# Performance work log

Hardware: AMD Instinct MI355X
Metric: run time of the kernel (lower is better)

Reference implementation:

```python
import jax, jax.numpy as jnp
import numpy as np

THETA = 10000.0


def _apply_rope(xh, positions, theta):
    # xh: [B, H, S, d_k]; positions: [S] int
    d_k = xh.shape[-1]
    inv_freq = theta ** (-jnp.arange(0, d_k, 2, dtype=jnp.float32) / d_k)  # [d_k/2]
    angles = positions.astype(jnp.float32)[:, None] * inv_freq[None, :]     # [S, d_k/2]
    cos = jnp.cos(angles)
    sin = jnp.sin(angles)
    x1 = xh[..., 0::2]
    x2 = xh[..., 1::2]
    r1 = x1 * cos - x2 * sin
    r2 = x1 * sin + x2 * cos
    return jnp.stack([r1, r2], axis=-1).reshape(xh.shape)


def setup_inputs() -> dict:
    key = jax.random.key(0)
    ks = jax.random.split(key, 5)
    B, S, D = 2, 2048, 1024
    std = np.sqrt(1.0 / D).astype(np.float32)
    return {
        "x": jax.random.normal(ks[0], (B, S, D), dtype=jnp.float32),
        "token_positions": jnp.arange(S, dtype=jnp.int64 if jax.config.jax_enable_x64 else jnp.int32),
        "Wq": jax.random.normal(ks[1], (D, D), dtype=jnp.float32) * std,
        "Wk": jax.random.normal(ks[2], (D, D), dtype=jnp.float32) * std,
        "Wv": jax.random.normal(ks[3], (D, D), dtype=jnp.float32) * std,
        "Wo": jax.random.normal(ks[4], (D, D), dtype=jnp.float32) * std,
    }


def reference(x, token_positions, Wq, Wk, Wv, Wo):
    B, S, D = x.shape
    n_heads = 16
    d_k = D // n_heads

    # QKV projections (torch does x @ W.T)
    q = x @ Wq.T
    k = x @ Wk.T
    v = x @ Wv.T

    def split_heads(t):  # [B,S,D] -> [B,H,S,d_k]
        return t.reshape(B, S, n_heads, d_k).transpose(0, 2, 1, 3)

    qh = _apply_rope(split_heads(q), token_positions, THETA)
    kh = _apply_rope(split_heads(k), token_positions, THETA)
    vh = split_heads(v)

    scores = jnp.einsum("bhqd,bhkd->bhqk", qh, kh) / jnp.sqrt(jnp.float32(d_k))
    causal = jnp.tril(jnp.ones((S, S), dtype=bool))
    scores = jnp.where(causal, scores, -jnp.inf)
    attn = jax.nn.softmax(scores, axis=-1)

    out_h = jnp.einsum("bhqk,bhkd->bhqd", attn, vh)  # [B,H,S,d_k]
    out = out_h.transpose(0, 2, 1, 3).reshape(B, S, D)
    return out @ Wo.T
```

## Files before the change

kernel.cpp:

```cpp
#include <hip/hip_runtime.h>

typedef unsigned int u32;
typedef __attribute__((ext_vector_type(8))) short short8;
typedef __attribute__((ext_vector_type(4))) float f32x4;

__device__ __forceinline__ unsigned short f2bf(float f) {
  union { float f; u32 u; } x; x.f = f;
  u32 u = x.u;
  return (unsigned short)((u + 0x7fffu + ((u >> 16) & 1u)) >> 16);
}
__device__ __forceinline__ float bf2f(unsigned short b) {
  union { u32 u; float f; } x; x.u = ((u32)b) << 16;
  return x.f;
}
__device__ __forceinline__ f32x4 mfma_bf16(short8 a, short8 b, f32x4 c) {
  return __builtin_amdgcn_mfma_f32_16x16x32_bf16(a, b, c, 0, 0, 0);
}

typedef __attribute__((address_space(3))) unsigned int lds_u32;
typedef const __attribute__((address_space(1))) unsigned int glb_u32;
__device__ __forceinline__ void gload_lds16(const unsigned short* g, unsigned short* l) {
  __builtin_amdgcn_global_load_lds((glb_u32*)g, (lds_u32*)l, 16, 0, 0);
}

__global__ __launch_bounds__(256) void cvt_kernel(const float* __restrict__ src,
                                                  unsigned short* __restrict__ dst, int n4) {
  int i = blockIdx.x * 256 + threadIdx.x;
  if (i >= n4) return;
  float4 v = ((const float4*)src)[i];
  ushort4 o;
  o.x = f2bf(v.x); o.y = f2bf(v.y); o.z = f2bf(v.z); o.w = f2bf(v.w);
  ((ushort4*)dst)[i] = o;
}

__global__ __launch_bounds__(256) void cvt_w_kernel(const float* __restrict__ wq,
                                                    const float* __restrict__ wk,
                                                    const float* __restrict__ wv,
                                                    const float* __restrict__ wo,
                                                    unsigned short* __restrict__ dqkv,
                                                    unsigned short* __restrict__ dwo) {
  const int i = blockIdx.x * 256 + threadIdx.x;
  const int w = blockIdx.y;
  const float* src = (w == 0) ? wq : (w == 1) ? wk : (w == 2) ? wv : wo;
  unsigned short* dst = (w == 3) ? dwo : dqkv + (size_t)w * 1048576;
  float4 v = ((const float4*)src)[i];
  ushort4 o;
  o.x = f2bf(v.x); o.y = f2bf(v.y); o.z = f2bf(v.z); o.w = f2bf(v.w);
  ((ushort4*)dst)[i] = o;
}

__global__ __launch_bounds__(256) void gemm_qkv(const unsigned short* __restrict__ A,
                                                const unsigned short* __restrict__ B,
                                                unsigned short* __restrict__ qk,
                                                unsigned short* __restrict__ kk,
                                                unsigned short* __restrict__ vtm) {
  constexpr int K = 1024;
  __shared__ unsigned short As[128 * 32];
  __shared__ unsigned short Bs[128 * 32];
  const int tid = threadIdx.x;
  const int wave = tid >> 6, lane = tid & 63;
  const int l15 = lane & 15, quad = lane >> 4;
  const int wr = wave >> 1, wc = wave & 1;
  const int m0 = blockIdx.y * 128, n0 = blockIdx.x * 128;
  f32x4 acc[4][4] = {};
  const int srow = wave * 32 + (lane >> 2);
  const int scol = (lane & 3) * 8;
  const unsigned short* Ag0 = A + (size_t)(m0 + srow) * K + scol;
  const unsigned short* Ag1 = A + (size_t)(m0 + srow + 16) * K + scol;
  const unsigned short* Bg0 = B + (size_t)(n0 + srow) * K + scol;
  const unsigned short* Bg1 = B + (size_t)(n0 + srow + 16) * K + scol;
  unsigned short* Al0 = &As[wave * 1024];
  unsigned short* Al1 = &As[wave * 1024 + 512];
  unsigned short* Bl0 = &Bs[wave * 1024];
  unsigned short* Bl1 = &Bs[wave * 1024 + 512];
  for (int k0 = 0; k0 < K; k0 += 32) {
    __syncthreads();
    gload_lds16(Ag0 + k0, Al0);
    gload_lds16(Ag1 + k0, Al1);
    gload_lds16(Bg0 + k0, Bl0);
    gload_lds16(Bg1 + k0, Bl1);
    __syncthreads();
    short8 a[4], b[4];
#pragma unroll
    for (int i = 0; i < 4; ++i) a[i] = *(const short8*)&As[(wr * 64 + i * 16 + l15) * 32 + quad * 8];
#pragma unroll
    for (int j = 0; j < 4; ++j) b[j] = *(const short8*)&Bs[(wc * 64 + j * 16 + l15) * 32 + quad * 8];
#pragma unroll
    for (int i = 0; i < 4; ++i)
#pragma unroll
      for (int j = 0; j < 4; ++j) acc[i][j] = mfma_bf16(a[i], b[j], acc[i][j]);
  }
  const int proj = n0 >> 10;
  const int nn0 = (n0 & 1023) + wc * 64;
  if (proj < 2) {
    unsigned short* dst = (proj == 0) ? qk : kk;
#pragma unroll
    for (int i = 0; i < 4; ++i) {
      const int mb = m0 + wr * 64 + i * 16 + quad * 4;
#pragma unroll
      for (int j = 0; j < 4; ++j) {
        const int nn = nn0 + j * 16 + l15;
#pragma unroll
        for (int r = 0; r < 4; ++r) dst[(size_t)(mb + r) * 1024 + nn] = f2bf(acc[i][j][r]);
      }
    }
  } else {
#pragma unroll
    for (int i = 0; i < 4; ++i) {
      const int mb = m0 + wr * 64 + i * 16 + quad * 4;
      const int bb = mb >> 11, s = mb & 2047;
#pragma unroll
      for (int j = 0; j < 4; ++j) {
        const int nn = nn0 + j * 16 + l15;
        const int h = nn >> 6, d = nn & 63;
        ushort4 v4;
        v4.x = f2bf(acc[i][j][0]); v4.y = f2bf(acc[i][j][1]);
        v4.z = f2bf(acc[i][j][2]); v4.w = f2bf(acc[i][j][3]);
        *(ushort4*)&vtm[(((size_t)bb * 16 + h) * 64 + d) * 2048 + s] = v4;
      }
    }
  }
}

__global__ __launch_bounds__(256) void rope_kernel(unsigned short* __restrict__ q,
                                                   unsigned short* __restrict__ k,
                                                   const int* __restrict__ pos) {
  const int idx = blockIdx.x * 256 + threadIdx.x;
  const int i = idx & 31;
  const int h = (idx >> 5) & 15;
  const int s = (idx >> 9) & 2047;
  const int b = idx >> 20;
  const float p = (float)pos[s];
  const float inv = exp2f(-0.4152410118609203f * (float)i);
  float sn, cs;
  sincosf(p * inv, &sn, &cs);
  const size_t base = ((size_t)(b * 2048 + s)) * 1024 + h * 64 + 2 * i;
  {
    u32* qp = (u32*)(q + base);
    u32 w = *qp;
    float x1 = bf2f((unsigned short)(w & 0xffff)), x2 = bf2f((unsigned short)(w >> 16));
    *qp = (u32)f2bf(x1 * cs - x2 * sn) | ((u32)f2bf(x1 * sn + x2 * cs) << 16);
  }
  {
    u32* kp = (u32*)(k + base);
    u32 w = *kp;
    float x1 = bf2f((unsigned short)(w & 0xffff)), x2 = bf2f((unsigned short)(w >> 16));
    *kp = (u32)f2bf(x1 * cs - x2 * sn) | ((u32)f2bf(x1 * sn + x2 * cs) << 16);
  }
}

__global__ __launch_bounds__(64) void attn_kernel(const unsigned short* __restrict__ qk,
                                                  const unsigned short* __restrict__ kk,
                                                  const unsigned short* __restrict__ vtm,
                                                  unsigned short* __restrict__ om) {
  __shared__ unsigned short Pl[32 * 72];
  const int lane = threadIdx.x;
  const int l15 = lane & 15, quad = lane >> 4;
  const int bid = blockIdx.x;
  const int bh = bid & 31;
  const int qi = 63 - (bid >> 5);
  const int b = bh >> 4, h = bh & 15;
  const int qbase = qi << 5;
  const unsigned short* Qp = qk + (size_t)b * 2048 * 1024 + h * 64;
  const unsigned short* Kp = kk + (size_t)b * 2048 * 1024 + h * 64;
  const unsigned short* Vp = vtm + (size_t)bh * 64 * 2048;
  short8 qf[2][2];
#pragma unroll
  for (int f = 0; f < 2; ++f)
#pragma unroll
    for (int hh = 0; hh < 2; ++hh)
      qf[f][hh] = *(const short8*)(Qp + (size_t)(qbase + f * 16 + l15) * 1024 + hh * 32 + quad * 8);
  f32x4 o4[2][4] = {};
  f32x4 ls[2] = {};
  short8 ones;
#pragma unroll
  for (int j = 0; j < 8; ++j) ones[j] = (short)0x3F80;
  const float SC = 0.18033688011112042f;
  const int nk = (qbase + 95) >> 6;
  for (int kt = 0; kt < nk; ++kt) {
    const int kbase = kt << 6;
    short8 kb[4][2], vb[4][2];
#pragma unroll
    for (int nt = 0; nt < 4; ++nt)
#pragma unroll
      for (int hh = 0; hh < 2; ++hh)
        kb[nt][hh] = *(const short8*)(Kp + (size_t)(kbase + nt * 16 + l15) * 1024 + hh * 32 + quad * 8);
#pragma unroll
    for (int t = 0; t < 4; ++t)
#pragma unroll
      for (int hh = 0; hh < 2; ++hh)
        vb[t][hh] = *(const short8*)(Vp + (size_t)(t * 16 + l15) * 2048 + kbase + hh * 32 + quad * 8);
    f32x4 s4[2][4] = {};
#pragma unroll
    for (int f = 0; f < 2; ++f)
#pragma unroll
      for (int nt = 0; nt < 4; ++nt) {
        s4[f][nt] = mfma_bf16(qf[f][0], kb[nt][0], s4[f][nt]);
        s4[f][nt] = mfma_bf16(qf[f][1], kb[nt][1], s4[f][nt]);
      }
    const bool edge = (kt == nk - 1);
#pragma unroll
    for (int f = 0; f < 2; ++f) {
      const int row0 = qbase + f * 16 + quad * 4;
#pragma unroll
      for (int nt = 0; nt < 4; ++nt) {
        const int col = kbase + nt * 16 + l15;
#pragma unroll
        for (int r = 0; r < 4; ++r) {
          float p = exp2f(s4[f][nt][r] * SC);
          if (edge && col > row0 + r) p = 0.f;
          Pl[(f * 16 + quad * 4 + r) * 72 + nt * 16 + l15] = f2bf(p);
        }
      }
    }
    __asm volatile("s_waitcnt lgkmcnt(0)" ::: "memory");
    short8 pa[2][2];
#pragma unroll
    for (int f = 0; f < 2; ++f)
#pragma unroll
      for (int hh = 0; hh < 2; ++hh)
        pa[f][hh] = *(const short8*)&Pl[(f * 16 + l15) * 72 + hh * 32 + quad * 8];
#pragma unroll
    for (int f = 0; f < 2; ++f) {
#pragma unroll
      for (int t = 0; t < 4; ++t) {
        o4[f][t] = mfma_bf16(pa[f][0], vb[t][0], o4[f][t]);
        o4[f][t] = mfma_bf16(pa[f][1], vb[t][1], o4[f][t]);
      }
      ls[f] = mfma_bf16(pa[f][0], ones, ls[f]);
      ls[f] = mfma_bf16(pa[f][1], ones, ls[f]);
    }
  }
#pragma unroll
  for (int f = 0; f < 2; ++f) {
    f32x4 rl;
#pragma unroll
    for (int r = 0; r < 4; ++r) rl[r] = 1.f / ls[f][r];
#pragma unroll
    for (int t = 0; t < 4; ++t)
#pragma unroll
      for (int r = 0; r < 4; ++r) {
        const int srow = qbase + f * 16 + quad * 4 + r;
        om[((size_t)b * 2048 + srow) * 1024 + h * 64 + t * 16 + l15] = f2bf(o4[f][t][r] * rl[r]);
      }
  }
}

__global__ __launch_bounds__(256) void gemm_out(const unsigned short* __restrict__ A,
                                                const unsigned short* __restrict__ B,
                                                float* __restrict__ C) {
  constexpr int K = 1024;
  __shared__ unsigned short As[64 * 32];
  __shared__ unsigned short Bs[128 * 32];
  const int tid = threadIdx.x;
  const int wave = tid >> 6, lane = tid & 63;
  const int l15 = lane & 15, quad = lane >> 4;
  const int m0 = blockIdx.y * 64, n0 = blockIdx.x * 128;
  f32x4 acc[4][2] = {};
  const int lr = lane >> 2, lc = (lane & 3) * 8;
  const unsigned short* Ag  = A + (size_t)(m0 + wave * 16 + lr) * K + lc;
  const unsigned short* Bg0 = B + (size_t)(n0 + wave * 32 + lr) * K + lc;
  const unsigned short* Bg1 = B + (size_t)(n0 + wave * 32 + 16 + lr) * K + lc;
  unsigned short* Al  = &As[wave * 512];
  unsigned short* Bl0 = &Bs[wave * 1024];
  unsigned short* Bl1 = &Bs[wave * 1024 + 512];
  for (int k0 = 0; k0 < K; k0 += 32) {
    __syncthreads();
    gload_lds16(Ag + k0, Al);
    gload_lds16(Bg0 + k0, Bl0);
    gload_lds16(Bg1 + k0, Bl1);
    __syncthreads();
    short8 a[4], b[2];
#pragma unroll
    for (int i = 0; i < 4; ++i) a[i] = *(const short8*)&As[(i * 16 + l15) * 32 + quad * 8];
#pragma unroll
    for (int j = 0; j < 2; ++j) b[j] = *(const short8*)&Bs[(wave * 32 + j * 16 + l15) * 32 + quad * 8];
#pragma unroll
    for (int i = 0; i < 4; ++i)
#pragma unroll
      for (int j = 0; j < 2; ++j) acc[i][j] = mfma_bf16(a[i], b[j], acc[i][j]);
  }
#pragma unroll
  for (int i = 0; i < 4; ++i)
#pragma unroll
    for (int j = 0; j < 2; ++j)
#pragma unroll
      for (int r = 0; r < 4; ++r)
        C[(size_t)(m0 + i * 16 + quad * 4 + r) * 1024 + n0 + wave * 32 + j * 16 + l15] =
            acc[i][j][r];
}

extern "C" void kernel_launch(void* const* d_in, const int* in_sizes, int n_in,
                              void* d_out, int out_size, void* d_ws, size_t ws_size,
                              hipStream_t stream) {
  const float* x  = (const float*)d_in[0];
  const int* pos  = (const int*)d_in[1];
  const float* Wq = (const float*)d_in[2];
  const float* Wk = (const float*)d_in[3];
  const float* Wv = (const float*)d_in[4];
  const float* Wo = (const float*)d_in[5];
  float* out = (float*)d_out;
  char* ws = (char*)d_ws;
  unsigned short* xb   = (unsigned short*)(ws);
  unsigned short* wqkv = (unsigned short*)(ws + (size_t)( 8 << 20));
  unsigned short* wob  = (unsigned short*)(ws + (size_t)(14 << 20));
  unsigned short* qkb  = (unsigned short*)(ws + (size_t)(16 << 20));
  unsigned short* kkb  = (unsigned short*)(ws + (size_t)(24 << 20));
  unsigned short* vtm  = (unsigned short*)(ws + (size_t)(32 << 20));
  unsigned short* om   = (unsigned short*)(ws + (size_t)(40 << 20));

  const int NX4 = 4096 * 1024 / 4;
  hipLaunchKernelGGL(cvt_kernel, dim3(NX4 / 256), dim3(256), 0, stream, x, xb, NX4);
  hipLaunchKernelGGL(cvt_w_kernel, dim3(1024, 4), dim3(256), 0, stream, Wq, Wk, Wv, Wo, wqkv, wob);

  hipLaunchKernelGGL(gemm_qkv, dim3(24, 32), dim3(256), 0, stream, xb, wqkv, qkb, kkb, vtm);
  hipLaunchKernelGGL(rope_kernel, dim3(8192), dim3(256), 0, stream, qkb, kkb, pos);
  hipLaunchKernelGGL(attn_kernel, dim3(2048), dim3(64), 0, stream, qkb, kkb, vtm, om);
  hipLaunchKernelGGL(gemm_out, dim3(8, 64), dim3(256), 0, stream, om, wob, out);
}
```

Measured before the change: 237.7 us.

## Split key range across two waves per attention block and combine partials in LDS

Each attention block now runs two waves, each processing half of the causal key tiles for the same 32 query rows, then wave 1 writes its unnormalized output and row-sum accumulators to shared memory for wave 0 to add and normalize. This shortens the serial key loop per block and doubles the waves available to hide memory latency. It adds two block barriers, an LDS exchange, and idle time when the halves are unequal.

```diff
diff --git a/kernel.cpp b/kernel.cpp
--- a/kernel.cpp
+++ b/kernel.cpp
@@ -149,13 +149,15 @@
   }
 }
 
-__global__ __launch_bounds__(64) void attn_kernel(const unsigned short* __restrict__ qk,
-                                                  const unsigned short* __restrict__ kk,
-                                                  const unsigned short* __restrict__ vtm,
-                                                  unsigned short* __restrict__ om) {
-  __shared__ unsigned short Pl[32 * 72];
-  const int lane = threadIdx.x;
+__global__ __launch_bounds__(128, 4) void attn_kernel(const unsigned short* __restrict__ qk,
+                                                      const unsigned short* __restrict__ kk,
+                                                      const unsigned short* __restrict__ vtm,
+                                                      unsigned short* __restrict__ om) {
+  __shared__ f32x4 cmb[640];
+  const int tid = threadIdx.x;
+  const int wave = tid >> 6, lane = tid & 63;
   const int l15 = lane & 15, quad = lane >> 4;
+  unsigned short* Pl = (unsigned short*)cmb + wave * 2304;
   const int bid = blockIdx.x;
   const int bh = bid & 31;
   const int qi = 63 - (bid >> 5);
@@ -177,7 +179,10 @@
   for (int j = 0; j < 8; ++j) ones[j] = (short)0x3F80;
   const float SC = 0.18033688011112042f;
   const int nk = (qbase + 95) >> 6;
-  for (int kt = 0; kt < nk; ++kt) {
+  const int half = (nk + 1) >> 1;
+  const int k0w = wave * half;
+  const int k1w = (wave == 0) ? half : nk;
+  for (int kt = k0w; kt < k1w; ++kt) {
     const int kbase = kt << 6;
     short8 kb[4][2], vb[4][2];
 #pragma unroll
@@ -231,18 +236,34 @@
       ls[f] = mfma_bf16(pa[f][1], ones, ls[f]);
     }
   }
-#pragma unroll
-  for (int f = 0; f < 2; ++f) {
-    f32x4 rl;
-#pragma unroll
-    for (int r = 0; r < 4; ++r) rl[r] = 1.f / ls[f][r];
-#pragma unroll
-    for (int t = 0; t < 4; ++t)
-#pragma unroll
-      for (int r = 0; r < 4; ++r) {
-        const int srow = qbase + f * 16 + quad * 4 + r;
-        om[((size_t)b * 2048 + srow) * 1024 + h * 64 + t * 16 + l15] = f2bf(o4[f][t][r] * rl[r]);
-      }
+  __syncthreads();
+  if (wave == 1) {
+#pragma unroll
+    for (int f = 0; f < 2; ++f) {
+#pragma unroll
+      for (int t = 0; t < 4; ++t) cmb[(f * 4 + t) * 64 + lane] = o4[f][t];
+      cmb[512 + f * 64 + lane] = ls[f];
+    }
+  }
+  __syncthreads();
+  if (wave == 0) {
+#pragma unroll
+    for (int f = 0; f < 2; ++f) {
+      f32x4 lw = cmb[512 + f * 64 + lane];
+      f32x4 lt;
+#pragma unroll
+      for (int r = 0; r < 4; ++r) lt[r] = 1.f / (ls[f][r] + lw[r]);
+#pragma unroll
+      for (int t = 0; t < 4; ++t) {
+        f32x4 ow = cmb[(f * 4 + t) * 64 + lane];
+#pragma unroll
+        for (int r = 0; r < 4; ++r) {
+          const int srow = qbase + f * 16 + quad * 4 + r;
+          om[((size_t)b * 2048 + srow) * 1024 + h * 64 + t * 16 + l15] =
+              f2bf((o4[f][t][r] + ow[r]) * lt[r]);
+        }
+      }
+    }
   }
 }
 
@@ -315,6 +336,6 @@
 
   hipLaunchKernelGGL(gemm_qkv, dim3(24, 32), dim3(256), 0, stream, xb, wqkv, qkb, kkb, vtm);
   hipLaunchKernelGGL(rope_kernel, dim3(8192), dim3(256), 0, stream, qkb, kkb, pos);
-  hipLaunchKernelGGL(attn_kernel, dim3(2048), dim3(64), 0, stream, qkb, kkb, vtm, om);
+  hipLaunchKernelGGL(attn_kernel, dim3(2048), dim3(128), 0, stream, qkb, kkb, vtm, om);
   hipLaunchKernelGGL(gemm_out, dim3(8, 64), dim3(256), 0, stream, om, wob, out);
 }
```

Result: slower. 264.7 us (+11.4%).

## Split attention KV range across two blocks and combine partial outputs

Applied to the files above, without the earlier changes.

Adds a split-K attention variant in which each query tile's key range is divided into two halves handled by separate blocks. Each block writes unnormalized fp32 partial outputs and row sums, and a combine kernel adds them and normalizes into bf16. The aim is more parallelism and better load balance across CUs for the causal workload. The cost is an extra kernel launch and about 32MB of fp32 intermediate traffic. It relies on exp2 without max subtraction, matching the existing kernel's numerics, and only runs when the workspace is large enough.

```diff
diff --git a/kernel.cpp b/kernel.cpp
--- a/kernel.cpp
+++ b/kernel.cpp
@@ -149,6 +149,135 @@
   }
 }
 
+__global__ __launch_bounds__(64, 4) void attn_split(const unsigned short* __restrict__ qk,
+                                                    const unsigned short* __restrict__ kk,
+                                                    const unsigned short* __restrict__ vtm,
+                                                    float* __restrict__ op,
+                                                    float* __restrict__ lsum) {
+  __shared__ unsigned short Pl[32 * 72];
+  const int lane = threadIdx.x;
+  const int l15 = lane & 15, quad = lane >> 4;
+  const int bid = blockIdx.x;
+  const int split = bid >> 11;
+  const int rem = bid & 2047;
+  const int bh = rem & 31;
+  const int qi = 63 - (rem >> 5);
+  const int b = bh >> 4, h = bh & 15;
+  const int qbase = qi << 5;
+  const unsigned short* Qp = qk + (size_t)b * 2048 * 1024 + h * 64;
+  const unsigned short* Kp = kk + (size_t)b * 2048 * 1024 + h * 64;
+  const unsigned short* Vp = vtm + (size_t)bh * 64 * 2048;
+  short8 qf[2][2];
+#pragma unroll
+  for (int f = 0; f < 2; ++f)
+#pragma unroll
+    for (int hh = 0; hh < 2; ++hh)
+      qf[f][hh] = *(const short8*)(Qp + (size_t)(qbase + f * 16 + l15) * 1024 + hh * 32 + quad * 8);
+  f32x4 o4[2][4] = {};
+  f32x4 ls[2] = {};
+  short8 ones;
+#pragma unroll
+  for (int j = 0; j < 8; ++j) ones[j] = (short)0x3F80;
+  const float SC = 0.18033688011112042f;
+  const int nk = (qbase + 95) >> 6;
+  const int half = (nk + 1) >> 1;
+  const int kts = split * half;
+  const int kte = split ? nk : half;
+  for (int kt = kts; kt < kte; ++kt) {
+    const int kbase = kt << 6;
+    short8 kb[4][2], vb[4][2];
+#pragma unroll
+    for (int nt = 0; nt < 4; ++nt)
+#pragma unroll
+      for (int hh = 0; hh < 2; ++hh)
+        kb[nt][hh] = *(const short8*)(Kp + (size_t)(kbase + nt * 16 + l15) * 1024 + hh * 32 + quad * 8);
+#pragma unroll
+    for (int t = 0; t < 4; ++t)
+#pragma unroll
+      for (int hh = 0; hh < 2; ++hh)
+        vb[t][hh] = *(const short8*)(Vp + (size_t)(t * 16 + l15) * 2048 + kbase + hh * 32 + quad * 8);
+    f32x4 s4[2][4] = {};
+#pragma unroll
+    for (int f = 0; f < 2; ++f)
+#pragma unroll
+      for (int nt = 0; nt < 4; ++nt) {
+        s4[f][nt] = mfma_bf16(qf[f][0], kb[nt][0], s4[f][nt]);
+        s4[f][nt] = mfma_bf16(qf[f][1], kb[nt][1], s4[f][nt]);
+      }
+    const bool edge = (kt == nk - 1);
+#pragma unroll
+    for (int f = 0; f < 2; ++f) {
+      const int row0 = qbase + f * 16 + quad * 4;
+#pragma unroll
+      for (int nt = 0; nt < 4; ++nt) {
+        const int col = kbase + nt * 16 + l15;
+#pragma unroll
+        for (int r = 0; r < 4; ++r) {
+          float p = exp2f(s4[f][nt][r] * SC);
+          if (edge && col > row0 + r) p = 0.f;
+          Pl[(f * 16 + quad * 4 + r) * 72 + nt * 16 + l15] = f2bf(p);
+        }
+      }
+    }
+    __asm volatile("s_waitcnt lgkmcnt(0)" ::: "memory");
+    short8 pa[2][2];
+#pragma unroll
+    for (int f = 0; f < 2; ++f)
+#pragma unroll
+      for (int hh = 0; hh < 2; ++hh)
+        pa[f][hh] = *(const short8*)&Pl[(f * 16 + l15) * 72 + hh * 32 + quad * 8];
+#pragma unroll
+    for (int f = 0; f < 2; ++f) {
+#pragma unroll
+      for (int t = 0; t < 4; ++t) {
+        o4[f][t] = mfma_bf16(pa[f][0], vb[t][0], o4[f][t]);
+        o4[f][t] = mfma_bf16(pa[f][1], vb[t][1], o4[f][t]);
+      }
+      ls[f] = mfma_bf16(pa[f][0], ones, ls[f]);
+      ls[f] = mfma_bf16(pa[f][1], ones, ls[f]);
+    }
+  }
+  float* opp = op + (size_t)split * 4096 * 1024;
+#pragma unroll
+  for (int f = 0; f < 2; ++f)
+#pragma unroll
+    for (int t = 0; t < 4; ++t)
+#pragma unroll
+      for (int r = 0; r < 4; ++r) {
+        const int srow = qbase + f * 16 + quad * 4 + r;
+        opp[((size_t)b * 2048 + srow) * 1024 + h * 64 + t * 16 + l15] = o4[f][t][r];
+      }
+  if (l15 == 0) {
+#pragma unroll
+    for (int f = 0; f < 2; ++f)
+#pragma unroll
+      for (int r = 0; r < 4; ++r) {
+        const int srow = qbase + f * 16 + quad * 4 + r;
+        lsum[((((size_t)split * 2 + b) * 16 + h) * 2048) + srow] = ls[f][r];
+      }
+  }
+}
+
+__global__ __launch_bounds__(256) void attn_combine(const float* __restrict__ op,
+                                                    const float* __restrict__ lsum,
+                                                    unsigned short* __restrict__ om) {
+  const int i = blockIdx.x * 256 + threadIdx.x;
+  const int row = i >> 8;
+  const int b = row >> 11, s = row & 2047;
+  const int h = (i & 255) >> 4;
+  float4 a0 = ((const float4*)op)[i];
+  float4 a1 = ((const float4*)(op + (size_t)4096 * 1024))[i];
+  const float l0 = lsum[((size_t)b * 16 + h) * 2048 + s];
+  const float l1 = lsum[(((size_t)2 + b) * 16 + h) * 2048 + s];
+  const float rl = 1.f / (l0 + l1);
+  ushort4 o;
+  o.x = f2bf((a0.x + a1.x) * rl);
+  o.y = f2bf((a0.y + a1.y) * rl);
+  o.z = f2bf((a0.z + a1.z) * rl);
+  o.w = f2bf((a0.w + a1.w) * rl);
+  ((ushort4*)om)[i] = o;
+}
+
 __global__ __launch_bounds__(64) void attn_kernel(const unsigned short* __restrict__ qk,
                                                   const unsigned short* __restrict__ kk,
                                                   const unsigned short* __restrict__ vtm,
@@ -308,6 +437,8 @@
   unsigned short* kkb  = (unsigned short*)(ws + (size_t)(24 << 20));
   unsigned short* vtm  = (unsigned short*)(ws + (size_t)(32 << 20));
   unsigned short* om   = (unsigned short*)(ws + (size_t)(40 << 20));
+  float* op   = (float*)(ws + (size_t)(48 << 20));
+  float* lsum = (float*)(ws + (size_t)(80 << 20));
 
   const int NX4 = 4096 * 1024 / 4;
   hipLaunchKernelGGL(cvt_kernel, dim3(NX4 / 256), dim3(256), 0, stream, x, xb, NX4);
@@ -315,6 +446,11 @@
 
   hipLaunchKernelGGL(gemm_qkv, dim3(24, 32), dim3(256), 0, stream, xb, wqkv, qkb, kkb, vtm);
   hipLaunchKernelGGL(rope_kernel, dim3(8192), dim3(256), 0, stream, qkb, kkb, pos);
-  hipLaunchKernelGGL(attn_kernel, dim3(2048), dim3(64), 0, stream, qkb, kkb, vtm, om);
+  if (ws_size >= ((size_t)81 << 20)) {
+    hipLaunchKernelGGL(attn_split, dim3(4096), dim3(64), 0, stream, qkb, kkb, vtm, op, lsum);
+    hipLaunchKernelGGL(attn_combine, dim3(4096), dim3(256), 0, stream, op, lsum, om);
+  } else {
+    hipLaunchKernelGGL(attn_kernel, dim3(2048), dim3(64), 0, stream, qkb, kkb, vtm, om);
+  }
   hipLaunchKernelGGL(gemm_out, dim3(8, 64), dim3(256), 0, stream, om, wob, out);
 }
```

Result: slower. 245.8 us (+3.4%).

## Share K/V tiles across four waves via LDS in attention kernel

Applied to the files above, without the earlier changes.

The attention kernel now runs four waves per block, each handling a 32-row query slice of a 128-row block. They cooperatively load each 64-key K/V tile into XOR-swizzled shared memory with direct global-to-LDS loads, instead of every wave fetching K/V from global memory on its own. This cuts redundant global/L2 traffic by four. In exchange it adds two block barriers per tile and fewer blocks, and waves whose causal range has ended sit idle while the block's last tiles are processed.

```diff
diff --git a/kernel.cpp b/kernel.cpp
--- a/kernel.cpp
+++ b/kernel.cpp
@@ -149,18 +149,22 @@
   }
 }
 
-__global__ __launch_bounds__(64) void attn_kernel(const unsigned short* __restrict__ qk,
-                                                  const unsigned short* __restrict__ kk,
-                                                  const unsigned short* __restrict__ vtm,
-                                                  unsigned short* __restrict__ om) {
-  __shared__ unsigned short Pl[32 * 72];
-  const int lane = threadIdx.x;
+__global__ __launch_bounds__(256) void attn_shared(const unsigned short* __restrict__ qk,
+                                                   const unsigned short* __restrict__ kk,
+                                                   const unsigned short* __restrict__ vtm,
+                                                   unsigned short* __restrict__ om) {
+  __shared__ unsigned short Ks[64 * 64];
+  __shared__ unsigned short Vs[64 * 64];
+  __shared__ unsigned short PlA[4][32 * 72];
+  const int tid = threadIdx.x;
+  const int wave = tid >> 6, lane = tid & 63;
   const int l15 = lane & 15, quad = lane >> 4;
+  unsigned short* Pl = PlA[wave];
   const int bid = blockIdx.x;
   const int bh = bid & 31;
-  const int qi = 63 - (bid >> 5);
+  const int qblk = 15 - (bid >> 5);
   const int b = bh >> 4, h = bh & 15;
-  const int qbase = qi << 5;
+  const int qbase = qblk * 128 + wave * 32;
   const unsigned short* Qp = qk + (size_t)b * 2048 * 1024 + h * 64;
   const unsigned short* Kp = kk + (size_t)b * 2048 * 1024 + h * 64;
   const unsigned short* Vp = vtm + (size_t)bh * 64 * 2048;
@@ -176,59 +180,78 @@
 #pragma unroll
   for (int j = 0; j < 8; ++j) ones[j] = (short)0x3F80;
   const float SC = 0.18033688011112042f;
-  const int nk = (qbase + 95) >> 6;
-  for (int kt = 0; kt < nk; ++kt) {
+  const int nkb = (qblk * 128 + 191) >> 6;
+  const int nkw = (qbase + 95) >> 6;
+  const int srow = wave * 16 + (lane >> 3);
+  const int scs = (((lane & 7) ^ (srow & 7)) * 8);
+  const unsigned short* KgB = Kp + (size_t)srow * 1024 + scs;
+  const unsigned short* VgB = Vp + (size_t)srow * 2048 + scs;
+  unsigned short* Kl0 = &Ks[(wave * 16) * 64];
+  unsigned short* Kl1 = &Ks[(wave * 16 + 8) * 64];
+  unsigned short* Vl0 = &Vs[(wave * 16) * 64];
+  unsigned short* Vl1 = &Vs[(wave * 16 + 8) * 64];
+  const int sw0 = ((quad ^ (l15 & 7)) * 8);
+  const int sw1 = (((4 + quad) ^ (l15 & 7)) * 8);
+  for (int kt = 0; kt < nkb; ++kt) {
     const int kbase = kt << 6;
-    short8 kb[4][2], vb[4][2];
-#pragma unroll
-    for (int nt = 0; nt < 4; ++nt)
-#pragma unroll
-      for (int hh = 0; hh < 2; ++hh)
-        kb[nt][hh] = *(const short8*)(Kp + (size_t)(kbase + nt * 16 + l15) * 1024 + hh * 32 + quad * 8);
-#pragma unroll
-    for (int t = 0; t < 4; ++t)
-#pragma unroll
-      for (int hh = 0; hh < 2; ++hh)
-        vb[t][hh] = *(const short8*)(Vp + (size_t)(t * 16 + l15) * 2048 + kbase + hh * 32 + quad * 8);
-    f32x4 s4[2][4] = {};
-#pragma unroll
-    for (int f = 0; f < 2; ++f)
+    __syncthreads();
+    gload_lds16(KgB + (size_t)kbase * 1024, Kl0);
+    gload_lds16(KgB + (size_t)kbase * 1024 + 8 * 1024, Kl1);
+    gload_lds16(VgB + kbase, Vl0);
+    gload_lds16(VgB + kbase + 8 * 2048, Vl1);
+    __syncthreads();
+    if (kt < nkw) {
+      short8 kb[4][2], vb[4][2];
 #pragma unroll
       for (int nt = 0; nt < 4; ++nt) {
-        s4[f][nt] = mfma_bf16(qf[f][0], kb[nt][0], s4[f][nt]);
-        s4[f][nt] = mfma_bf16(qf[f][1], kb[nt][1], s4[f][nt]);
-      }
-    const bool edge = (kt == nk - 1);
-#pragma unroll
-    for (int f = 0; f < 2; ++f) {
-      const int row0 = qbase + f * 16 + quad * 4;
-#pragma unroll
-      for (int nt = 0; nt < 4; ++nt) {
-        const int col = kbase + nt * 16 + l15;
-#pragma unroll
-        for (int r = 0; r < 4; ++r) {
-          float p = exp2f(s4[f][nt][r] * SC);
-          if (edge && col > row0 + r) p = 0.f;
-          Pl[(f * 16 + quad * 4 + r) * 72 + nt * 16 + l15] = f2bf(p);
+        kb[nt][0] = *(const short8*)&Ks[(nt * 16 + l15) * 64 + sw0];
+        kb[nt][1] = *(const short8*)&Ks[(nt * 16 + l15) * 64 + sw1];
+      }
+#pragma unroll
+      for (int t = 0; t < 4; ++t) {
+        vb[t][0] = *(const short8*)&Vs[(t * 16 + l15) * 64 + sw0];
+        vb[t][1] = *(const short8*)&Vs[(t * 16 + l15) * 64 + sw1];
+      }
+      f32x4 s4[2][4] = {};
+#pragma unroll
+      for (int f = 0; f < 2; ++f)
+#pragma unroll
+        for (int nt = 0; nt < 4; ++nt) {
+          s4[f][nt] = mfma_bf16(qf[f][0], kb[nt][0], s4[f][nt]);
+          s4[f][nt] = mfma_bf16(qf[f][1], kb[nt][1], s4[f][nt]);
         }
-      }
-    }
-    __asm volatile("s_waitcnt lgkmcnt(0)" ::: "memory");
-    short8 pa[2][2];
-#pragma unroll
-    for (int f = 0; f < 2; ++f)
-#pragma unroll
-      for (int hh = 0; hh < 2; ++hh)
-        pa[f][hh] = *(const short8*)&Pl[(f * 16 + l15) * 72 + hh * 32 + quad * 8];
-#pragma unroll
-    for (int f = 0; f < 2; ++f) {
-#pragma unroll
-      for (int t = 0; t < 4; ++t) {
-        o4[f][t] = mfma_bf16(pa[f][0], vb[t][0], o4[f][t]);
-        o4[f][t] = mfma_bf16(pa[f][1], vb[t][1], o4[f][t]);
-      }
-      ls[f] = mfma_bf16(pa[f][0], ones, ls[f]);
-      ls[f] = mfma_bf16(pa[f][1], ones, ls[f]);
+      const bool edge = (kbase + 63 > qbase);
+#pragma unroll
+      for (int f = 0; f < 2; ++f) {
+        const int row0 = qbase + f * 16 + quad * 4;
+#pragma unroll
+        for (int nt = 0; nt < 4; ++nt) {
+          const int col = kbase + nt * 16 + l15;
+#pragma unroll
+          for (int r = 0; r < 4; ++r) {
+            float p = exp2f(s4[f][nt][r] * SC);
+            if (edge && col > row0 + r) p = 0.f;
+            Pl[(f * 16 + quad * 4 + r) * 72 + nt * 16 + l15] = f2bf(p);
+          }
+        }
+      }
+      __asm volatile("s_waitcnt lgkmcnt(0)" ::: "memory");
+      short8 pa[2][2];
+#pragma unroll
+      for (int f = 0; f < 2; ++f)
+#pragma unroll
+        for (int hh = 0; hh < 2; ++hh)
+          pa[f][hh] = *(const short8*)&Pl[(f * 16 + l15) * 72 + hh * 32 + quad * 8];
+#pragma unroll
+      for (int f = 0; f < 2; ++f) {
+#pragma unroll
+        for (int t = 0; t < 4; ++t) {
+          o4[f][t] = mfma_bf16(pa[f][0], vb[t][0], o4[f][t]);
+          o4[f][t] = mfma_bf16(pa[f][1], vb[t][1], o4[f][t]);
+        }
+        ls[f] = mfma_bf16(pa[f][0], ones, ls[f]);
+        ls[f] = mfma_bf16(pa[f][1], ones, ls[f]);
+      }
     }
   }
 #pragma unroll
@@ -240,8 +263,8 @@
     for (int t = 0; t < 4; ++t)
 #pragma unroll
       for (int r = 0; r < 4; ++r) {
-        const int srow = qbase + f * 16 + quad * 4 + r;
-        om[((size_t)b * 2048 + srow) * 1024 + h * 64 + t * 16 + l15] = f2bf(o4[f][t][r] * rl[r]);
+        const int srw = qbase + f * 16 + quad * 4 + r;
+        om[((size_t)b * 2048 + srw) * 1024 + h * 64 + t * 16 + l15] = f2bf(o4[f][t][r] * rl[r]);
       }
   }
 }
@@ -315,6 +338,6 @@
 
   hipLaunchKernelGGL(gemm_qkv, dim3(24, 32), dim3(256), 0, stream, xb, wqkv, qkb, kkb, vtm);
   hipLaunchKernelGGL(rope_kernel, dim3(8192), dim3(256), 0, stream, qkb, kkb, pos);
-  hipLaunchKernelGGL(attn_kernel, dim3(2048), dim3(64), 0, stream, qkb, kkb, vtm, om);
+  hipLaunchKernelGGL(attn_shared, dim3(512), dim3(256), 0, stream, qkb, kkb, vtm, om);
   hipLaunchKernelGGL(gemm_out, dim3(8, 64), dim3(256), 0, stream, om, wob, out);
 }
```

Measured after the change: 231.1 us. 2.8% less time.
